# Optimization experiments

Measured on AMD Instinct MI355X. Metric: run time of the kernel, lower is better.

Reference implementation:

```python
import jax, jax.numpy as jnp
import numpy as np


def setup_inputs() -> dict:
    key = jax.random.key(0)
    k1, k2, k3, k4 = jax.random.split(key, 4)
    B, C, H, W = 2, 3, 160, 160
    n, L, s, k = 3000, 72, 4, 5
    return {
        "x": jax.random.normal(k1, (B, C, H, W), dtype=jnp.float32),
        "queries": jax.random.normal(k2, (B, L, H, W), dtype=jnp.float32),
        "keys": jax.random.normal(k3, (n, L), dtype=jnp.float32),
        "values": jax.random.normal(k4, (n, s * s, k * k), dtype=jnp.float32),
        "s": s,
        "k": k,
    }


def reference(x, queries, keys, values, s, k):
    B, C, H, W = x.shape
    pad = k // 2
    # reflect-pad spatial dims (matches F.pad mode='reflect')
    xp = jnp.pad(x, ((0, 0), (0, 0), (pad, pad), (pad, pad)), mode="reflect")
    # extract k*k patches: [B, C, H, W, k*k] (fixed small loop over k*k offsets)
    patches = jnp.stack(
        [xp[:, :, i : i + H, j : j + W] for i in range(k) for j in range(k)],
        axis=-1,
    )
    # per-pixel top-1 routing over codebook keys
    q = queries.transpose(0, 2, 3, 1)  # [B, H, W, L]
    sim = jnp.einsum("bhwl,nl->bhwn", q, keys)  # [B, H, W, n]
    idx = jnp.argmax(sim, axis=-1)  # [B, H, W] int
    v = values[idx]  # gather per-pixel kernel: [B, H, W, s^2, k^2]
    # per-pixel dynamic conv: [B, C, s^2, H, W]
    out = jnp.einsum("bchwk,bhwsk->bcshw", patches, v)
    # pixel shuffle with upscale s: [B, C, s^2, H, W] -> [B, C, H*s, W*s]
    out = out.reshape(B, C, s, s, H, W)
    out = out.transpose(0, 1, 4, 2, 5, 3)  # [B, C, H, s, W, s]
    return out.reshape(B, C, H * s, W * s)
```

## Files before the change

kernel.cpp:

```cpp
#include <hip/hip_runtime.h>

#define H 160
#define W 160
#define HW 25600
#define BB 2
#define CC 3
#define LL 72
#define NKEYS 3000
#define NKPAD 3008
#define NT 94
#define NG 47
#define NPIX (BB * HW)

#define CERR 3e-5f
#define ABSG 1e-3f

typedef __attribute__((ext_vector_type(8))) short bf8v;
typedef __attribute__((ext_vector_type(16))) float f16v;

union FU { uint4 u4; bf8v v; };

#define WS_KFRAG 1024
#define WS_LIST  963584
#define WS_IDX   1168384

__device__ inline unsigned bf16rn(float f) {
    unsigned u = __float_as_uint(f);
    return (u + 0x7FFFu + ((u >> 16) & 1u)) >> 16;
}

__global__ __launch_bounds__(64) void kprep_kernel(
    const float* __restrict__ keys, unsigned* __restrict__ ctrl,
    uint4* __restrict__ kfg)
{
    const int tile = blockIdx.x;
    const int lane = threadIdx.x;
    const int key  = tile * 32 + (lane & 31);
    const int half = lane >> 5;
    const bool kv  = (key < NKEYS);
    float kmax = 0.f;
#pragma unroll
    for (int ks = 0; ks < 5; ++ks) {
        unsigned wh[4], wl[4];
#pragma unroll
        for (int j = 0; j < 4; ++j) {
            const int l0 = ks * 16 + half * 8 + 2 * j;
            float v0 = (kv && l0     < LL) ? keys[(size_t)key * LL + l0]     : 0.f;
            float v1 = (kv && l0 + 1 < LL) ? keys[(size_t)key * LL + l0 + 1] : 0.f;
            kmax = fmaxf(kmax, fmaxf(fabsf(v0), fabsf(v1)));
            unsigned h0 = bf16rn(v0), h1 = bf16rn(v1);
            float r0 = v0 - __uint_as_float(h0 << 16);
            float r1 = v1 - __uint_as_float(h1 << 16);
            wh[j] = h0 | (h1 << 16);
            wl[j] = bf16rn(r0) | (bf16rn(r1) << 16);
        }
        const int base = tile * 640 + (ks * 2) * 64 + lane;
        kfg[base]      = make_uint4(wh[0], wh[1], wh[2], wh[3]);
        kfg[base + 64] = make_uint4(wl[0], wl[1], wl[2], wl[3]);
    }
#pragma unroll
    for (int m = 32; m >= 1; m >>= 1)
        kmax = fmaxf(kmax, __shfl_xor(kmax, m));
    if (lane == 0) atomicMax(&ctrl[1], __float_as_uint(kmax));
}

template<bool LAST>
__device__ inline void do_tile(const uint4* __restrict__ kb, int t, int tileIdx,
                               const FU* __restrict__ qh, const FU* __restrict__ ql,
                               int lane, int hb, float& b1, float& b2, int& bi)
{
    f16v acc;
#pragma unroll
    for (int r = 0; r < 16; ++r) acc[r] = 0.f;
#pragma unroll
    for (int ks = 0; ks < 5; ++ks) {
        FU kh, kl;
        kh.u4 = kb[(t * 5 + ks) * 128 + lane];
        kl.u4 = kb[(t * 5 + ks) * 128 + 64 + lane];
        acc = __builtin_amdgcn_mfma_f32_32x32x16_bf16(kh.v, qh[ks].v, acc, 0, 0, 0);
        acc = __builtin_amdgcn_mfma_f32_32x32x16_bf16(kh.v, ql[ks].v, acc, 0, 0, 0);
        acc = __builtin_amdgcn_mfma_f32_32x32x16_bf16(kl.v, qh[ks].v, acc, 0, 0, 0);
    }
    const int kb0 = tileIdx * 32 + hb;
    const int NR = LAST ? 12 : 16;
#pragma unroll
    for (int r = 0; r < NR; ++r) {
        const float s = acc[r];
        const int key = kb0 + ((r & 3) + 8 * (r >> 2));
        const bool gt = (s > b1);
        b2 = fmaxf(b2, fminf(s, b1));
        b1 = fmaxf(b1, s);
        bi = gt ? key : bi;
    }
}

__global__ __launch_bounds__(256) void route_kernel(
    const float* __restrict__ queries,
    const uint4* __restrict__ kfg,
    unsigned* __restrict__ ctrl,
    unsigned* __restrict__ list,
    int* __restrict__ idx_buf)
{
    __shared__ uint4 kbuf[2][1280];

    const int tid  = threadIdx.x;
    const int lane = tid & 63;
    const int wid  = tid >> 6;
    const int hv   = lane >> 5;
    const int hb   = 4 * hv;
    const int pbase = blockIdx.x * 128 + wid * 32;
    const int p    = pbase + (lane & 31);
    const int b    = p / HW;
    const int hw   = p - b * HW;
    const float* __restrict__ qp = queries + (size_t)b * LL * HW + hw;

    FU qh[5], ql[5];
    float Ssum = 0.f;
#pragma unroll
    for (int ks = 0; ks < 5; ++ks) {
        unsigned wh[4], wl[4];
#pragma unroll
        for (int j = 0; j < 4; ++j) {
            const int l0 = ks * 16 + hv * 8 + 2 * j;
            float v0 = (l0     < LL) ? qp[(size_t)l0 * HW]       : 0.f;
            float v1 = (l0 + 1 < LL) ? qp[(size_t)(l0 + 1) * HW] : 0.f;
            Ssum += fabsf(v0) + fabsf(v1);
            unsigned h0 = bf16rn(v0), h1 = bf16rn(v1);
            float r0 = v0 - __uint_as_float(h0 << 16);
            float r1 = v1 - __uint_as_float(h1 << 16);
            wh[j] = h0 | (h1 << 16);
            wl[j] = bf16rn(r0) | (bf16rn(r1) << 16);
        }
        qh[ks].u4 = make_uint4(wh[0], wh[1], wh[2], wh[3]);
        ql[ks].u4 = make_uint4(wl[0], wl[1], wl[2], wl[3]);
    }
    const float S_p = Ssum + __shfl_xor(Ssum, 32);
    const float kmax = __uint_as_float(ctrl[1]);

    float b1 = -3.0e38f, b2 = -3.0e38f;
    int bi = 0;

#pragma unroll
    for (int j = 0; j < 5; ++j)
        kbuf[0][tid + j * 256] = kfg[tid + j * 256];
    __syncthreads();

    for (int g = 0; g < NG; ++g) {
        const int cur = g & 1;
        if (g < NG - 1) {
#pragma unroll
            for (int j = 0; j < 5; ++j)
                kbuf[cur ^ 1][tid + j * 256] = kfg[(size_t)(g + 1) * 1280 + tid + j * 256];
        }
        const uint4* kb = kbuf[cur];
        do_tile<false>(kb, 0, 2 * g, qh, ql, lane, hb, b1, b2, bi);
        if (g == NG - 1) do_tile<true >(kb, 1, 2 * g + 1, qh, ql, lane, hb, b1, b2, bi);
        else             do_tile<false>(kb, 1, 2 * g + 1, qh, ql, lane, hb, b1, b2, bi);
        __syncthreads();
    }

    const float ob1 = __shfl_xor(b1, 32);
    const float ob2 = __shfl_xor(b2, 32);
    const int   obi = __shfl_xor(bi, 32);
    const float nb2 = fmaxf(fminf(b1, ob1), fmaxf(b2, ob2));
    const bool take = (ob1 > b1) || (ob1 == b1 && obi < bi);
    const float nb1 = fmaxf(b1, ob1);
    const int  nbi = take ? obi : bi;

    const float thr = 2.0f * (CERR * S_p * kmax + ABSG);
    const bool certain = ((nb1 - nb2) > thr);

    if ((lane & 32) == 0) {
        if (certain) idx_buf[p] = nbi;
        else { unsigned pos = atomicAdd(&ctrl[0], 1u); list[pos] = (unsigned)p; }
    }
}

__global__ __launch_bounds__(256) void cleanup_kernel(
    const float* __restrict__ queries, const float* __restrict__ keys,
    const unsigned* __restrict__ ctrl, const unsigned* __restrict__ list,
    int* __restrict__ idx_buf)
{
    __shared__ float qs[LL];
    __shared__ float rbest[4];
    __shared__ int   ridx[4];

    const int tid = threadIdx.x;
    const int ln  = tid & 63;
    const int wid = tid >> 6;
    const unsigned count = ctrl[0];

    for (unsigned u = blockIdx.x; u < count; u += gridDim.x) {
        const int p  = (int)list[u];
        const int b  = p / HW;
        const int hw = p - b * HW;

        __syncthreads();
        if (tid < LL)
            qs[tid] = queries[((size_t)b * LL + tid) * HW + hw];
        __syncthreads();

        float q[LL];
#pragma unroll
        for (int l = 0; l < LL; ++l) q[l] = qs[l];

        float best = -3.0e38f; int bidx = 0x7FFFFFFF;
#pragma unroll 1
        for (int it = 0; it < 12; ++it) {
            const int n  = it * 256 + tid;
            const int nc = (n < NKEYS) ? n : (NKEYS - 1);
            const float4* __restrict__ kr = (const float4*)(keys + (size_t)nc * LL);
            float a0 = 0.f, a1 = 0.f, a2 = 0.f, a3 = 0.f;
#pragma unroll
            for (int j = 0; j < 18; ++j) {
                float4 kv = kr[j];
                a0 = fmaf(q[4 * j + 0], kv.x, a0);
                a1 = fmaf(q[4 * j + 1], kv.y, a1);
                a2 = fmaf(q[4 * j + 2], kv.z, a2);
                a3 = fmaf(q[4 * j + 3], kv.w, a3);
            }
            const float s = (a0 + a1) + (a2 + a3);
            if (n < NKEYS && (s > best || (s == best && n < bidx))) { best = s; bidx = n; }
        }
#pragma unroll
        for (int m = 32; m >= 1; m >>= 1) {
            const float ob = __shfl_xor(best, m);
            const int   oi = __shfl_xor(bidx, m);
            if (ob > best || (ob == best && oi < bidx)) { best = ob; bidx = oi; }
        }
        if (ln == 0) { rbest[wid] = best; ridx[wid] = bidx; }
        __syncthreads();
        if (tid == 0) {
            float fb = rbest[0]; int fi = ridx[0];
#pragma unroll
            for (int wvi = 1; wvi < 4; ++wvi) {
                if (rbest[wvi] > fb || (rbest[wvi] == fb && ridx[wvi] < fi)) {
                    fb = rbest[wvi]; fi = ridx[wvi];
                }
            }
            idx_buf[p] = fi;
        }
    }
}

__global__ __launch_bounds__(256) void conv_kernel(
    const float* __restrict__ x,
    const float* __restrict__ values,
    const int* __restrict__ idx_buf,
    float* __restrict__ out)
{
    const int p  = blockIdx.x * 256 + threadIdx.x;
    const int b  = p / HW;
    const int hw = p - b * HW;
    const int h  = hw / W;
    const int w  = hw - h * W;

    const int idx = idx_buf[p];

    float patch[CC][25];
#pragma unroll
    for (int i = 0; i < 5; ++i) {
        int r = h + i - 2;
        r = (r < 0) ? -r : ((r >= H) ? (2 * H - 2 - r) : r);
#pragma unroll
        for (int j = 0; j < 5; ++j) {
            int cidx = w + j - 2;
            cidx = (cidx < 0) ? -cidx : ((cidx >= W) ? (2 * W - 2 - cidx) : cidx);
#pragma unroll
            for (int c = 0; c < CC; ++c)
                patch[c][i * 5 + j] = x[((size_t)(b * CC + c) * H + r) * W + cidx];
        }
    }

    const float* vbase = values + (size_t)idx * 400;
    float acc[CC][16];
#pragma unroll
    for (int c = 0; c < CC; ++c)
#pragma unroll
        for (int si = 0; si < 16; ++si) acc[c][si] = 0.f;

#pragma unroll
    for (int si = 0; si < 16; ++si) {
        float v[25];
#pragma unroll
        for (int kk = 0; kk < 25; ++kk) v[kk] = vbase[si * 25 + kk];
#pragma unroll
        for (int c = 0; c < CC; ++c) {
            float a = 0.f;
#pragma unroll
            for (int kk = 0; kk < 25; ++kk) a += patch[c][kk] * v[kk];
            acc[c][si] = a;
        }
    }

#pragma unroll
    for (int c = 0; c < CC; ++c) {
#pragma unroll
        for (int sy = 0; sy < 4; ++sy) {
            float4 o = make_float4(acc[c][sy * 4 + 0], acc[c][sy * 4 + 1],
                                   acc[c][sy * 4 + 2], acc[c][sy * 4 + 3]);
            size_t off = ((size_t)(b * CC + c) * (H * 4) + (h * 4 + sy)) * (size_t)(W * 4)
                         + (size_t)w * 4;
            *(float4*)(&out[off]) = o;
        }
    }
}

extern "C" void kernel_launch(void* const* d_in, const int* in_sizes, int n_in,
                              void* d_out, int out_size, void* d_ws, size_t ws_size,
                              hipStream_t stream) {
    const float* x       = (const float*)d_in[0];
    const float* queries = (const float*)d_in[1];
    const float* keys    = (const float*)d_in[2];
    const float* values  = (const float*)d_in[3];
    float* out = (float*)d_out;

    char* ws = (char*)d_ws;
    unsigned* ctrl   = (unsigned*)ws;
    uint4*    kfg    = (uint4*)(ws + WS_KFRAG);
    unsigned* list   = (unsigned*)(ws + WS_LIST);
    int*      idxb   = (int*)(ws + WS_IDX);

    hipMemsetAsync(d_ws, 0, 8, stream);
    kprep_kernel<<<NT, 64, 0, stream>>>(keys, ctrl, kfg);
    route_kernel<<<NPIX / 128, 256, 0, stream>>>(queries, kfg, ctrl, list, idxb);
    cleanup_kernel<<<2048, 256, 0, stream>>>(queries, keys, ctrl, list, idxb);
    conv_kernel<<<NPIX / 256, 256, 0, stream>>>(x, values, idxb, out);
}
```

Measured before the change: 150.4 us.

## Split key range across blocks and process two pixel tiles per wave

The routing kernel now handles 64 pixels per wave, two 32-pixel MFMA tiles sharing each key fragment load from LDS. The key dimension is split four ways across blockIdx.y, so each block scans about a quarter of the keys. Partial top-2 results go to workspace, and a new combine kernel merges them and decides between a certain result and cleanup. It also uses fmed3 for the second-best update. This doubles fragment register use and adds one kernel launch plus partial-result traffic, in exchange for more reuse of each LDS key read and a larger grid that should fill the GPU better.

```diff
diff --git a/kernel.cpp b/kernel.cpp
--- a/kernel.cpp
+++ b/kernel.cpp
@@ -7,9 +7,8 @@
 #define CC 3
 #define LL 72
 #define NKEYS 3000
-#define NKPAD 3008
 #define NT 94
-#define NG 47
+#define NSPL 4
 #define NPIX (BB * HW)
 
 #define CERR 3e-5f
@@ -21,8 +20,12 @@
 union FU { uint4 u4; bf8v v; };
 
 #define WS_KFRAG 1024
-#define WS_LIST  963584
-#define WS_IDX   1168384
+#define WS_B1    963584
+#define WS_B2    1782784
+#define WS_BI    2601984
+#define WS_THR   3421184
+#define WS_LIST  3625984
+#define WS_IDX   3830784
 
 __device__ inline unsigned bf16rn(float f) {
     unsigned u = __float_as_uint(f);
@@ -64,58 +67,10 @@
     if (lane == 0) atomicMax(&ctrl[1], __float_as_uint(kmax));
 }
 
-template<bool LAST>
-__device__ inline void do_tile(const uint4* __restrict__ kb, int t, int tileIdx,
-                               const FU* __restrict__ qh, const FU* __restrict__ ql,
-                               int lane, int hb, float& b1, float& b2, int& bi)
-{
-    f16v acc;
-#pragma unroll
-    for (int r = 0; r < 16; ++r) acc[r] = 0.f;
-#pragma unroll
-    for (int ks = 0; ks < 5; ++ks) {
-        FU kh, kl;
-        kh.u4 = kb[(t * 5 + ks) * 128 + lane];
-        kl.u4 = kb[(t * 5 + ks) * 128 + 64 + lane];
-        acc = __builtin_amdgcn_mfma_f32_32x32x16_bf16(kh.v, qh[ks].v, acc, 0, 0, 0);
-        acc = __builtin_amdgcn_mfma_f32_32x32x16_bf16(kh.v, ql[ks].v, acc, 0, 0, 0);
-        acc = __builtin_amdgcn_mfma_f32_32x32x16_bf16(kl.v, qh[ks].v, acc, 0, 0, 0);
-    }
-    const int kb0 = tileIdx * 32 + hb;
-    const int NR = LAST ? 12 : 16;
-#pragma unroll
-    for (int r = 0; r < NR; ++r) {
-        const float s = acc[r];
-        const int key = kb0 + ((r & 3) + 8 * (r >> 2));
-        const bool gt = (s > b1);
-        b2 = fmaxf(b2, fminf(s, b1));
-        b1 = fmaxf(b1, s);
-        bi = gt ? key : bi;
-    }
-}
-
-__global__ __launch_bounds__(256) void route_kernel(
-    const float* __restrict__ queries,
-    const uint4* __restrict__ kfg,
-    unsigned* __restrict__ ctrl,
-    unsigned* __restrict__ list,
-    int* __restrict__ idx_buf)
-{
-    __shared__ uint4 kbuf[2][1280];
-
-    const int tid  = threadIdx.x;
-    const int lane = tid & 63;
-    const int wid  = tid >> 6;
-    const int hv   = lane >> 5;
-    const int hb   = 4 * hv;
-    const int pbase = blockIdx.x * 128 + wid * 32;
-    const int p    = pbase + (lane & 31);
-    const int b    = p / HW;
-    const int hw   = p - b * HW;
-    const float* __restrict__ qp = queries + (size_t)b * LL * HW + hw;
-
-    FU qh[5], ql[5];
-    float Ssum = 0.f;
+__device__ __forceinline__ void build_qfrag(
+    const float* __restrict__ qp, int hv, FU* qh, FU* ql, float& Ssum)
+{
+    Ssum = 0.f;
 #pragma unroll
     for (int ks = 0; ks < 5; ++ks) {
         unsigned wh[4], wl[4];
@@ -134,46 +89,157 @@
         qh[ks].u4 = make_uint4(wh[0], wh[1], wh[2], wh[3]);
         ql[ks].u4 = make_uint4(wl[0], wl[1], wl[2], wl[3]);
     }
-    const float S_p = Ssum + __shfl_xor(Ssum, 32);
-    const float kmax = __uint_as_float(ctrl[1]);
-
-    float b1 = -3.0e38f, b2 = -3.0e38f;
-    int bi = 0;
+}
+
+template<bool LAST>
+__device__ __forceinline__ void do_tile2(
+    const uint4* __restrict__ kb, int t, int tileIdx,
+    const FU* __restrict__ qhA, const FU* __restrict__ qlA,
+    const FU* __restrict__ qhB, const FU* __restrict__ qlB,
+    int lane, int hb,
+    float& b1A, float& b2A, int& biA,
+    float& b1B, float& b2B, int& biB)
+{
+    f16v accA, accB;
+#pragma unroll
+    for (int r = 0; r < 16; ++r) { accA[r] = 0.f; accB[r] = 0.f; }
+#pragma unroll
+    for (int ks = 0; ks < 5; ++ks) {
+        FU kh, kl;
+        kh.u4 = kb[(t * 5 + ks) * 128 + lane];
+        kl.u4 = kb[(t * 5 + ks) * 128 + 64 + lane];
+        accA = __builtin_amdgcn_mfma_f32_32x32x16_bf16(kh.v, qhA[ks].v, accA, 0, 0, 0);
+        accB = __builtin_amdgcn_mfma_f32_32x32x16_bf16(kh.v, qhB[ks].v, accB, 0, 0, 0);
+        accA = __builtin_amdgcn_mfma_f32_32x32x16_bf16(kh.v, qlA[ks].v, accA, 0, 0, 0);
+        accB = __builtin_amdgcn_mfma_f32_32x32x16_bf16(kh.v, qlB[ks].v, accB, 0, 0, 0);
+        accA = __builtin_amdgcn_mfma_f32_32x32x16_bf16(kl.v, qhA[ks].v, accA, 0, 0, 0);
+        accB = __builtin_amdgcn_mfma_f32_32x32x16_bf16(kl.v, qhB[ks].v, accB, 0, 0, 0);
+    }
+    const int kb0 = tileIdx * 32 + hb;
+    const int NR = LAST ? 12 : 16;
+#pragma unroll
+    for (int r = 0; r < NR; ++r) {
+        const int key = kb0 + ((r & 3) + 8 * (r >> 2));
+        {
+            const float s = accA[r];
+            const float n2 = __builtin_amdgcn_fmed3f(b1A, b2A, s);
+            const bool gt = (s > b1A);
+            b1A = fmaxf(b1A, s); b2A = n2; biA = gt ? key : biA;
+        }
+        {
+            const float s = accB[r];
+            const float n2 = __builtin_amdgcn_fmed3f(b1B, b2B, s);
+            const bool gt = (s > b1B);
+            b1B = fmaxf(b1B, s); b2B = n2; biB = gt ? key : biB;
+        }
+    }
+}
+
+__global__ __launch_bounds__(256, 2) void route_kernel(
+    const float* __restrict__ queries,
+    const uint4* __restrict__ kfg,
+    const unsigned* __restrict__ ctrl,
+    float* __restrict__ b1s, float* __restrict__ b2s,
+    int* __restrict__ bis, float* __restrict__ thr)
+{
+    __shared__ uint4 kbuf[2][1280];
+
+    const int tid   = threadIdx.x;
+    const int lane  = tid & 63;
+    const int wid   = tid >> 6;
+    const int hv    = lane >> 5;
+    const int hb    = 4 * hv;
+    const int split = blockIdx.y;
+    const int pA = blockIdx.x * 256 + wid * 64 + (lane & 31);
+    const int pB = pA + 32;
+
+    FU qhA[5], qlA[5], qhB[5], qlB[5];
+    float SsA, SsB;
+    {
+        const int bA = pA / HW, hwA = pA - bA * HW;
+        build_qfrag(queries + (size_t)bA * LL * HW + hwA, hv, qhA, qlA, SsA);
+        const int bB = pB / HW, hwB = pB - bB * HW;
+        build_qfrag(queries + (size_t)bB * LL * HW + hwB, hv, qhB, qlB, SsB);
+    }
+
+    float b1A = -3.0e38f, b2A = -3.0e38f; int biA = 0;
+    float b1B = -3.0e38f, b2B = -3.0e38f; int biB = 0;
+
+    const int t0 = split * 24;
+    const int ng = (split == NSPL - 1) ? 11 : 12;
 
 #pragma unroll
     for (int j = 0; j < 5; ++j)
-        kbuf[0][tid + j * 256] = kfg[tid + j * 256];
+        kbuf[0][tid + j * 256] = kfg[(size_t)t0 * 640 + tid + j * 256];
     __syncthreads();
 
-    for (int g = 0; g < NG; ++g) {
+    for (int g = 0; g < ng; ++g) {
         const int cur = g & 1;
-        if (g < NG - 1) {
+        if (g < ng - 1) {
 #pragma unroll
             for (int j = 0; j < 5; ++j)
-                kbuf[cur ^ 1][tid + j * 256] = kfg[(size_t)(g + 1) * 1280 + tid + j * 256];
+                kbuf[cur ^ 1][tid + j * 256] =
+                    kfg[(size_t)(t0 + 2 * (g + 1)) * 640 + tid + j * 256];
         }
         const uint4* kb = kbuf[cur];
-        do_tile<false>(kb, 0, 2 * g, qh, ql, lane, hb, b1, b2, bi);
-        if (g == NG - 1) do_tile<true >(kb, 1, 2 * g + 1, qh, ql, lane, hb, b1, b2, bi);
-        else             do_tile<false>(kb, 1, 2 * g + 1, qh, ql, lane, hb, b1, b2, bi);
+        const int base = t0 + 2 * g;
+        do_tile2<false>(kb, 0, base, qhA, qlA, qhB, qlB, lane, hb,
+                        b1A, b2A, biA, b1B, b2B, biB);
+        if (base + 1 == NT - 1)
+            do_tile2<true >(kb, 1, base + 1, qhA, qlA, qhB, qlB, lane, hb,
+                            b1A, b2A, biA, b1B, b2B, biB);
+        else
+            do_tile2<false>(kb, 1, base + 1, qhA, qlA, qhB, qlB, lane, hb,
+                            b1A, b2A, biA, b1B, b2B, biB);
         __syncthreads();
     }
 
-    const float ob1 = __shfl_xor(b1, 32);
-    const float ob2 = __shfl_xor(b2, 32);
-    const int   obi = __shfl_xor(bi, 32);
-    const float nb2 = fmaxf(fminf(b1, ob1), fmaxf(b2, ob2));
-    const bool take = (ob1 > b1) || (ob1 == b1 && obi < bi);
-    const float nb1 = fmaxf(b1, ob1);
-    const int  nbi = take ? obi : bi;
-
-    const float thr = 2.0f * (CERR * S_p * kmax + ABSG);
-    const bool certain = ((nb1 - nb2) > thr);
+    const float o1A = __shfl_xor(b1A, 32), o2A = __shfl_xor(b2A, 32);
+    const int   oiA = __shfl_xor(biA, 32);
+    const float n2A = fmaxf(fminf(b1A, o1A), fmaxf(b2A, o2A));
+    const bool  tkA = (o1A > b1A) || (o1A == b1A && oiA < biA);
+    const float n1A = fmaxf(b1A, o1A);
+    const int   niA = tkA ? oiA : biA;
+
+    const float o1B = __shfl_xor(b1B, 32), o2B = __shfl_xor(b2B, 32);
+    const int   oiB = __shfl_xor(biB, 32);
+    const float n2B = fmaxf(fminf(b1B, o1B), fmaxf(b2B, o2B));
+    const bool  tkB = (o1B > b1B) || (o1B == b1B && oiB < biB);
+    const float n1B = fmaxf(b1B, o1B);
+    const int   niB = tkB ? oiB : biB;
 
     if ((lane & 32) == 0) {
-        if (certain) idx_buf[p] = nbi;
-        else { unsigned pos = atomicAdd(&ctrl[0], 1u); list[pos] = (unsigned)p; }
-    }
+        const int sp = split * NPIX;
+        b1s[sp + pA] = n1A; b2s[sp + pA] = n2A; bis[sp + pA] = niA;
+        b1s[sp + pB] = n1B; b2s[sp + pB] = n2B; bis[sp + pB] = niB;
+        if (split == 0) {
+            const float kmax = __uint_as_float(ctrl[1]);
+            const float SpA = SsA + __shfl_xor(SsA, 32);
+            const float SpB = SsB + __shfl_xor(SsB, 32);
+            thr[pA] = 2.0f * (CERR * SpA * kmax + ABSG);
+            thr[pB] = 2.0f * (CERR * SpB * kmax + ABSG);
+        }
+    }
+}
+
+__global__ __launch_bounds__(256) void combine_kernel(
+    const float* __restrict__ b1s, const float* __restrict__ b2s,
+    const int* __restrict__ bis, const float* __restrict__ thr,
+    unsigned* __restrict__ ctrl, unsigned* __restrict__ list,
+    int* __restrict__ idx_buf)
+{
+    const int p = blockIdx.x * 256 + threadIdx.x;
+    float m1 = -3.0e38f, m2 = -3.0e38f; int bi = 0;
+#pragma unroll
+    for (int s = 0; s < NSPL; ++s) {
+        const float a1 = b1s[s * NPIX + p];
+        const float a2 = b2s[s * NPIX + p];
+        const int   ai = bis[s * NPIX + p];
+        if (a1 > m1) { m2 = fmaxf(m1, a2); m1 = a1; bi = ai; }
+        else         { m2 = fmaxf(m2, a1); }
+    }
+    if ((m1 - m2) > thr[p]) idx_buf[p] = bi;
+    else { unsigned pos = atomicAdd(&ctrl[0], 1u); list[pos] = (unsigned)p; }
 }
 
 __global__ __launch_bounds__(256) void cleanup_kernel(
@@ -316,14 +382,20 @@
     float* out = (float*)d_out;
 
     char* ws = (char*)d_ws;
-    unsigned* ctrl   = (unsigned*)ws;
-    uint4*    kfg    = (uint4*)(ws + WS_KFRAG);
-    unsigned* list   = (unsigned*)(ws + WS_LIST);
-    int*      idxb   = (int*)(ws + WS_IDX);
+    unsigned* ctrl = (unsigned*)ws;
+    uint4*    kfg  = (uint4*)(ws + WS_KFRAG);
+    float*    b1s  = (float*)(ws + WS_B1);
+    float*    b2s  = (float*)(ws + WS_B2);
+    int*      bis  = (int*)(ws + WS_BI);
+    float*    thr  = (float*)(ws + WS_THR);
+    unsigned* list = (unsigned*)(ws + WS_LIST);
+    int*      idxb = (int*)(ws + WS_IDX);
 
     hipMemsetAsync(d_ws, 0, 8, stream);
     kprep_kernel<<<NT, 64, 0, stream>>>(keys, ctrl, kfg);
-    route_kernel<<<NPIX / 128, 256, 0, stream>>>(queries, kfg, ctrl, list, idxb);
+    route_kernel<<<dim3(NPIX / 256, NSPL), 256, 0, stream>>>(queries, kfg, ctrl,
+                                                             b1s, b2s, bis, thr);
+    combine_kernel<<<NPIX / 256, 256, 0, stream>>>(b1s, b2s, bis, thr, ctrl, list, idxb);
     cleanup_kernel<<<2048, 256, 0, stream>>>(queries, keys, ctrl, list, idxb);
     conv_kernel<<<NPIX / 256, 256, 0, stream>>>(x, values, idxb, out);
 }
```

Measured after the change: 145.8 us. 3.1% less time.
